# Optimization experiments

Hardware: AMD Instinct MI355X
Metric: run time of the kernel (lower is better)

The kernel has to match this reference:

```python
import jax, jax.numpy as jnp
import numpy as np

# Model dims (match init_kwargs)
E, D, H, K = 8, 512, 1024, 2   # num_experts, input/output dim, hidden dim, top_k
B, S = 4, 2048                 # batch, seq_len


def setup_inputs() -> dict:
    key = jax.random.key(0)
    ks = jax.random.split(key, 5)
    sd = lambda fan: np.float32(1.0 / np.sqrt(fan))
    return {
        "x": jax.random.normal(ks[0], (B, S, D), jnp.float32),
        "gate_w": jax.random.normal(ks[1], (D, E), jnp.float32) * sd(D),
        "gate_b": jnp.zeros((E,), jnp.float32),
        "w1": jax.random.normal(ks[2], (E, D, H), jnp.float32) * sd(D),
        "b1": jnp.zeros((E, H), jnp.float32),
        "w2": jax.random.normal(ks[3], (E, H, D), jnp.float32) * sd(H),
        "b2": jnp.zeros((E, D), jnp.float32),
    }


def reference(x, gate_w, gate_b, w1, b1, w2, b2):
    # x: [B, S, D]
    Bb, Ss, Dd = x.shape
    xf = x.reshape(-1, Dd)                              # [N, D], N = B*S

    # Router: softmax over experts, top-k, renormalize selected weights
    logits = xf @ gate_w + gate_b                        # [N, E]
    probs = jax.nn.softmax(logits, axis=-1)              # [N, E]
    top_w, top_i = jax.lax.top_k(probs, K)               # [N, K]
    top_w = top_w / top_w.sum(axis=-1, keepdims=True)

    # Per-token combine weight for each expert (0 if not routed).
    onehot = jax.nn.one_hot(top_i, E, dtype=probs.dtype)  # [N, K, E]
    combine = jnp.einsum("nke,nk->ne", onehot, top_w)     # [N, E]

    # Expert MLPs. Dropout is inactive at inference (identity).
    # h: [E, N, H]; GELU exact (torch nn.GELU default uses erf)
    h = jax.nn.gelu(jnp.einsum("nd,edh->enh", xf, w1) + b1[:, None, :],
                    approximate=False)
    y = jnp.einsum("enh,ehd->end", h, w2) + b2[:, None, :]  # [E, N, D]

    # Weighted combine: tokens not routed to expert e have combine[:, e] == 0.
    out = jnp.einsum("end,ne->nd", y, combine).reshape(Bb, Ss, Dd)
    return out, probs.reshape(Bb, Ss, E)
```

## Files before the change

kernel.cpp:

```cpp
#include <hip/hip_runtime.h>
#include <stdint.h>

#define N_TOK 8192
#define DIM   512
#define HID   1024
#define NE    8
#define NSLOT 16384
#define MAXSLOT 17408

typedef __attribute__((ext_vector_type(8))) short short8;
typedef __attribute__((ext_vector_type(4))) float f32x4;

#define W1T_OFF  0ull
#define W2T_OFF  8388608ull
#define H_OFF    16777216ull
#define Y_OFF    52428800ull
#define XBF_OFF  52428800ull
#define TOPI_OFF 70254592ull
#define TOPW_OFF 70320128ull
#define SLOT_OFF 70385664ull
#define ROWS_OFF 70451200ull
#define RW_OFF   70520832ull
#define CNT_OFF  70590464ull

__device__ __forceinline__ unsigned int f2bfu(float f) {
  union { float f; unsigned int i; } v; v.f = f;
  unsigned int u = v.i;
  return (u + 0x7FFFu + ((u >> 16) & 1u)) >> 16;
}
__device__ __forceinline__ float bf2f(unsigned int u) {
  union { unsigned int i; float f; } v; v.i = (u & 0xFFFFu) << 16; return v.f;
}
__device__ __forceinline__ float gelu_f(float x) {
  float x2 = x * x;
  float u = x * (1.59576912f + 0.07135481f * x2);
  float ez = __expf(-u);
  return x * __builtin_amdgcn_rcpf(1.0f + ez);
}
__device__ __forceinline__ void async16(void* lds, const void* g) {
  __builtin_amdgcn_global_load_lds(
      (const __attribute__((address_space(1))) unsigned int*)g,
      (__attribute__((address_space(3))) unsigned int*)lds, 16, 0, 0);
}

__global__ __launch_bounds__(256) void k_transpose(
    const float* __restrict__ w1, const float* __restrict__ w2,
    unsigned short* __restrict__ w1t, unsigned short* __restrict__ w2t) {
  __shared__ unsigned short tile[64][68];
  int b = blockIdx.x, tid = threadIdx.x;
  const float* src; unsigned short* dst; int R, C;
  if (b < 1024) { int e = b >> 7; int t = b & 127;
    src = w1 + (size_t)e * 524288; dst = w1t + (size_t)e * 524288; R = 512; C = 1024;
    int tr = t >> 4, tc = t & 15;
    src += (size_t)tr * 64 * C + tc * 64; dst += (size_t)tc * 64 * R + tr * 64;
  } else { b -= 1024; int e = b >> 7; int t = b & 127;
    src = w2 + (size_t)e * 524288; dst = w2t + (size_t)e * 524288; R = 1024; C = 512;
    int tr = t >> 3, tc = t & 7;
    src += (size_t)tr * 64 * C + tc * 64; dst += (size_t)tc * 64 * R + tr * 64;
  }
#pragma unroll
  for (int i = 0; i < 4; ++i) {
    int l = i * 256 + tid;
    int r = l >> 4, c4 = (l & 15) << 2;
    float4 v = *(const float4*)(src + (size_t)r * C + c4);
    tile[r][c4 + 0] = (unsigned short)f2bfu(v.x);
    tile[r][c4 + 1] = (unsigned short)f2bfu(v.y);
    tile[r][c4 + 2] = (unsigned short)f2bfu(v.z);
    tile[r][c4 + 3] = (unsigned short)f2bfu(v.w);
  }
  __syncthreads();
#pragma unroll
  for (int i = 0; i < 2; ++i) {
    int l = i * 256 + tid;
    int rr = l >> 3, c8 = (l & 7) << 3;
    ushort4 a, b2v;
    a.x = tile[c8 + 0][rr]; a.y = tile[c8 + 1][rr];
    a.z = tile[c8 + 2][rr]; a.w = tile[c8 + 3][rr];
    b2v.x = tile[c8 + 4][rr]; b2v.y = tile[c8 + 5][rr];
    b2v.z = tile[c8 + 6][rr]; b2v.w = tile[c8 + 7][rr];
    uint4 pk;
    pk.x = (unsigned int)a.x | ((unsigned int)a.y << 16);
    pk.y = (unsigned int)a.z | ((unsigned int)a.w << 16);
    pk.z = (unsigned int)b2v.x | ((unsigned int)b2v.y << 16);
    pk.w = (unsigned int)b2v.z | ((unsigned int)b2v.w << 16);
    *(uint4*)(dst + (size_t)rr * R + c8) = pk;
  }
}

__global__ __launch_bounds__(256) void k_router(
    const float* __restrict__ x, const float* __restrict__ gw,
    const float* __restrict__ gb, float* __restrict__ probs_out,
    int2* __restrict__ topi, float2* __restrict__ topw,
    unsigned short* __restrict__ xbf) {
  int wave = threadIdx.x >> 6, lane = threadIdx.x & 63;
  int n = blockIdx.x * 4 + wave;
  const float4* xr = (const float4*)(x + (size_t)n * DIM);
  float4 x0 = xr[lane * 2], x1 = xr[lane * 2 + 1];
  float xf[8] = {x0.x, x0.y, x0.z, x0.w, x1.x, x1.y, x1.z, x1.w};
  uint4 pa;
  pa.x = f2bfu(xf[0]) | (f2bfu(xf[1]) << 16);
  pa.y = f2bfu(xf[2]) | (f2bfu(xf[3]) << 16);
  pa.z = f2bfu(xf[4]) | (f2bfu(xf[5]) << 16);
  pa.w = f2bfu(xf[6]) | (f2bfu(xf[7]) << 16);
  *(uint4*)(xbf + (size_t)n * DIM + lane * 8) = pa;
  float acc[8] = {0.f,0.f,0.f,0.f,0.f,0.f,0.f,0.f};
  const float4* gwr = (const float4*)gw;
#pragma unroll
  for (int j = 0; j < 8; ++j) {
    int d = lane * 8 + j;
    float4 g0 = gwr[d * 2], g1 = gwr[d * 2 + 1];
    acc[0] += xf[j] * g0.x; acc[1] += xf[j] * g0.y; acc[2] += xf[j] * g0.z; acc[3] += xf[j] * g0.w;
    acc[4] += xf[j] * g1.x; acc[5] += xf[j] * g1.y; acc[6] += xf[j] * g1.z; acc[7] += xf[j] * g1.w;
  }
#pragma unroll
  for (int o = 1; o < 64; o <<= 1)
#pragma unroll
    for (int e = 0; e < 8; ++e) acc[e] += __shfl_xor(acc[e], o, 64);
  float p[8], mx = -1e30f, s = 0.f;
#pragma unroll
  for (int e = 0; e < 8; ++e) { p[e] = acc[e] + gb[e]; mx = fmaxf(mx, p[e]); }
#pragma unroll
  for (int e = 0; e < 8; ++e) { p[e] = __expf(p[e] - mx); s += p[e]; }
  float inv = 1.f / s;
#pragma unroll
  for (int e = 0; e < 8; ++e) p[e] *= inv;
  if (lane < 8) probs_out[(size_t)n * NE + lane] = p[lane];
  if (lane == 0) {
    int i0 = 0; float v0 = p[0];
#pragma unroll
    for (int e = 1; e < 8; ++e) if (p[e] > v0) { v0 = p[e]; i0 = e; }
    int i1 = -1; float v1 = -1.f;
#pragma unroll
    for (int e = 0; e < 8; ++e) if (e != i0 && p[e] > v1) { v1 = p[e]; i1 = e; }
    float sw = 1.f / (v0 + v1);
    topi[n] = make_int2(i0, i1);
    topw[n] = make_float2(v0 * sw, v1 * sw);
  }
}

__global__ __launch_bounds__(1024) void k_count(
    const int2* __restrict__ topi, int* __restrict__ meta, int* __restrict__ chunk_base,
    int* __restrict__ rows, float* __restrict__ rw) {
  __shared__ int ch[32][8];
  __shared__ int tot[8], poff_s[9], tiles_s[8];
  int t = threadIdx.x;
  int g = t >> 5;
  if (t < 256) ((int*)ch)[t] = 0;
  __syncthreads();
  int c[8] = {0,0,0,0,0,0,0,0};
  int base_tok = t * 8;
#pragma unroll
  for (int i = 0; i < 8; ++i) {
    int2 e = topi[base_tok + i];
#pragma unroll
    for (int k = 0; k < 8; ++k) c[k] += (e.x == k) + (e.y == k);
  }
#pragma unroll
  for (int k = 0; k < 8; ++k) if (c[k]) atomicAdd(&ch[g][k], c[k]);
  __syncthreads();
  if (t < 8) {
    int a = 0;
#pragma unroll
    for (int b = 0; b < 32; ++b) { int v = ch[b][t]; ch[b][t] = a; a += v; }
    tot[t] = a; meta[t] = a;
  }
  __syncthreads();
  if (t == 0) {
    int a = 0, ts = 0;
#pragma unroll
    for (int e = 0; e < 8; ++e) {
      int tiles = (tot[e] + 127) >> 7;
      poff_s[e] = a; tiles_s[e] = tiles;
      meta[16 + e] = a; meta[32 + e] = ts;
      a += tiles << 7; ts += tiles;
    }
    poff_s[8] = a; meta[24] = a; meta[40] = ts;
  }
  __syncthreads();
  if (t < 256) {
    int b = t >> 3, e = t & 7;
    chunk_base[t] = poff_s[e] + ch[b][e];
  }
#pragma unroll
  for (int e = 0; e < 8; ++e) {
    int padn = (tiles_s[e] << 7) - tot[e];
    if (t < padn) {
      int s = poff_s[e] + tot[e] + t;
      rows[s] = 0; rw[s] = 0.f;
    }
  }
}

__global__ __launch_bounds__(256) void k_assign(
    const int2* __restrict__ topi, const float2* __restrict__ topw,
    const int* __restrict__ chunk_base,
    int* __restrict__ rows, float* __restrict__ rw, int* __restrict__ slot_of) {
  __shared__ int lcnt[8];
  __shared__ int lbase[8];
  int t = threadIdx.x, b = blockIdx.x;
  if (t < 8) { lcnt[t] = 0; lbase[t] = chunk_base[b * 8 + t]; }
  __syncthreads();
  int n = b * 256 + t;
  int2 ei = topi[n]; float2 wv = topw[n];
  int r0 = atomicAdd(&lcnt[ei.x], 1);
  int r1 = atomicAdd(&lcnt[ei.y], 1);
  int s0 = lbase[ei.x] + r0;
  int s1 = lbase[ei.y] + r1;
  rows[s0] = n; rw[s0] = wv.x; slot_of[2 * n] = s0;
  rows[s1] = n; rw[s1] = wv.y; slot_of[2 * n + 1] = s1;
}

__global__ __launch_bounds__(256) void k_gemm1(
    const unsigned short* __restrict__ xbf, const unsigned short* __restrict__ w1t,
    const float* __restrict__ b1, const int* __restrict__ meta,
    const int* __restrict__ rows, unsigned short* __restrict__ h) {
  int t = blockIdx.y;
  if (t >= meta[40]) return;
  int e = 0;
#pragma unroll
  for (int i = 1; i < 8; ++i) if (t >= meta[32 + i]) e = i;
  int mt = t - meta[32 + e];
  int row0 = meta[16 + e] + (mt << 7);
  int nt = blockIdx.x;
  __shared__ __align__(16) unsigned short As[2][4096];
  __shared__ __align__(16) unsigned short Bs[2][4096];
  int tid = threadIdx.x;
  int wave = tid >> 6, lane = tid & 63;
  int wr = wave & 1, wc = wave >> 1;
  f32x4 acc[4][4] = {};
  const unsigned short* bBase = w1t + (size_t)e * HID * DIM + (size_t)(nt * 128) * DIM;

  const unsigned short* ga[2]; const unsigned short* gb[2];
#pragma unroll
  for (int j = 0; j < 2; ++j) {
    int s = j * 256 + tid;
    int r = s >> 2;
    int cg = ((s & 3) ^ ((r >> 1) & 3)) << 3;
    ga[j] = xbf + (size_t)rows[row0 + r] * DIM + cg;
    gb[j] = bBase + (size_t)r * DIM + cg;
  }
  int ldst = (wave * 64) * 8;

#pragma unroll
  for (int j = 0; j < 2; ++j) {
    async16(&As[0][j * 2048 + ldst], ga[j]);
    async16(&Bs[0][j * 2048 + ldst], gb[j]);
  }
  __syncthreads();

  for (int k0 = 0; k0 < DIM; k0 += 32) {
    int cur = (k0 >> 5) & 1, nxt = cur ^ 1;
    if (k0 + 32 < DIM) {
#pragma unroll
      for (int j = 0; j < 2; ++j) {
        async16(&As[nxt][j * 2048 + ldst], ga[j] + k0 + 32);
        async16(&Bs[nxt][j * 2048 + ldst], gb[j] + k0 + 32);
      }
    }
    {
      int ca = lane >> 4;
      short8 tf[4], wf[4];
#pragma unroll
      for (int am = 0; am < 4; ++am) {
        int ra = wr * 64 + am * 16 + (lane & 15);
        tf[am] = *(const short8*)&As[cur][(ra * 4 + (ca ^ ((ra >> 1) & 3))) * 8];
      }
#pragma unroll
      for (int an = 0; an < 4; ++an) {
        int rb = wc * 64 + an * 16 + (lane & 15);
        wf[an] = *(const short8*)&Bs[cur][(rb * 4 + (ca ^ ((rb >> 1) & 3))) * 8];
      }
#pragma unroll
      for (int an = 0; an < 4; ++an)
#pragma unroll
        for (int am = 0; am < 4; ++am)
          acc[an][am] = __builtin_amdgcn_mfma_f32_16x16x32_bf16(wf[an], tf[am], acc[an][am], 0, 0, 0);
    }
    __syncthreads();
  }
  int ml = lane & 15, q = lane >> 4;
#pragma unroll
  for (int am = 0; am < 4; ++am) {
    int slot_r = row0 + wr * 64 + am * 16 + ml;
    unsigned short* hrow = h + (size_t)slot_r * HID;
#pragma unroll
    for (int an = 0; an < 4; ++an) {
      int colb = nt * 128 + wc * 64 + an * 16 + q * 4;
      float4 bias = *(const float4*)&b1[e * HID + colb];
      f32x4 v = acc[an][am];
      float g0 = gelu_f(v[0] + bias.x);
      float g1 = gelu_f(v[1] + bias.y);
      float g2 = gelu_f(v[2] + bias.z);
      float g3 = gelu_f(v[3] + bias.w);
      uint2 pk;
      pk.x = f2bfu(g0) | (f2bfu(g1) << 16);
      pk.y = f2bfu(g2) | (f2bfu(g3) << 16);
      *(uint2*)(hrow + colb) = pk;
    }
  }
}

__global__ __launch_bounds__(256) void k_gemm2(
    const unsigned short* __restrict__ h, const unsigned short* __restrict__ w2t,
    const float* __restrict__ b2, const int* __restrict__ meta,
    const float* __restrict__ rw, unsigned short* __restrict__ y) {
  int t = blockIdx.y;
  if (t >= meta[40]) return;
  int e = 0;
#pragma unroll
  for (int i = 1; i < 8; ++i) if (t >= meta[32 + i]) e = i;
  int mt = t - meta[32 + e];
  int row0 = meta[16 + e] + (mt << 7);
  int nt = blockIdx.x;
  __shared__ __align__(16) unsigned short As[2][4096];
  __shared__ __align__(16) unsigned short Bs[2][4096];
  int tid = threadIdx.x;
  int wave = tid >> 6, lane = tid & 63;
  int wr = wave & 1, wc = wave >> 1;
  f32x4 acc[4][4] = {};
  const unsigned short* aBase = h + (size_t)row0 * HID;
  const unsigned short* bBase = w2t + (size_t)e * DIM * HID + (size_t)(nt * 128) * HID;

  const unsigned short* ga[2]; const unsigned short* gb[2];
#pragma unroll
  for (int j = 0; j < 2; ++j) {
    int s = j * 256 + tid;
    int r = s >> 2;
    int cg = ((s & 3) ^ ((r >> 1) & 3)) << 3;
    ga[j] = aBase + (size_t)r * HID + cg;
    gb[j] = bBase + (size_t)r * HID + cg;
  }
  int ldst = (wave * 64) * 8;

#pragma unroll
  for (int j = 0; j < 2; ++j) {
    async16(&As[0][j * 2048 + ldst], ga[j]);
    async16(&Bs[0][j * 2048 + ldst], gb[j]);
  }
  __syncthreads();

  for (int k0 = 0; k0 < HID; k0 += 32) {
    int cur = (k0 >> 5) & 1, nxt = cur ^ 1;
    if (k0 + 32 < HID) {
#pragma unroll
      for (int j = 0; j < 2; ++j) {
        async16(&As[nxt][j * 2048 + ldst], ga[j] + k0 + 32);
        async16(&Bs[nxt][j * 2048 + ldst], gb[j] + k0 + 32);
      }
    }
    {
      int ca = lane >> 4;
      short8 tf[4], wf[4];
#pragma unroll
      for (int am = 0; am < 4; ++am) {
        int ra = wr * 64 + am * 16 + (lane & 15);
        tf[am] = *(const short8*)&As[cur][(ra * 4 + (ca ^ ((ra >> 1) & 3))) * 8];
      }
#pragma unroll
      for (int an = 0; an < 4; ++an) {
        int rb = wc * 64 + an * 16 + (lane & 15);
        wf[an] = *(const short8*)&Bs[cur][(rb * 4 + (ca ^ ((rb >> 1) & 3))) * 8];
      }
#pragma unroll
      for (int an = 0; an < 4; ++an)
#pragma unroll
        for (int am = 0; am < 4; ++am)
          acc[an][am] = __builtin_amdgcn_mfma_f32_16x16x32_bf16(wf[an], tf[am], acc[an][am], 0, 0, 0);
    }
    __syncthreads();
  }
  int ml = lane & 15, q = lane >> 4;
#pragma unroll
  for (int am = 0; am < 4; ++am) {
    int slot_r = row0 + wr * 64 + am * 16 + ml;
    float w = rw[slot_r];
    unsigned short* yrow = y + (size_t)slot_r * DIM;
#pragma unroll
    for (int an = 0; an < 4; ++an) {
      int colb = nt * 128 + wc * 64 + an * 16 + q * 4;
      float4 bias = *(const float4*)&b2[e * DIM + colb];
      f32x4 v = acc[an][am];
      uint2 pk;
      pk.x = f2bfu((v[0] + bias.x) * w) | (f2bfu((v[1] + bias.y) * w) << 16);
      pk.y = f2bfu((v[2] + bias.z) * w) | (f2bfu((v[3] + bias.w) * w) << 16);
      *(uint2*)(yrow + colb) = pk;
    }
  }
}

__global__ __launch_bounds__(256) void k_combine(
    const unsigned short* __restrict__ y, const int* __restrict__ slot_of,
    float* __restrict__ out) {
  int t = blockIdx.x * 256 + threadIdx.x;
  int n = t >> 6, c = (t & 63) << 3;
  int s0 = slot_of[2 * n], s1 = slot_of[2 * n + 1];
  uint4 u0 = *(const uint4*)(y + (size_t)s0 * DIM + c);
  uint4 u1 = *(const uint4*)(y + (size_t)s1 * DIM + c);
  float4 o0, o1;
  o0.x = bf2f(u0.x) + bf2f(u1.x); o0.y = bf2f(u0.x >> 16) + bf2f(u1.x >> 16);
  o0.z = bf2f(u0.y) + bf2f(u1.y); o0.w = bf2f(u0.y >> 16) + bf2f(u1.y >> 16);
  o1.x = bf2f(u0.z) + bf2f(u1.z); o1.y = bf2f(u0.z >> 16) + bf2f(u1.z >> 16);
  o1.z = bf2f(u0.w) + bf2f(u1.w); o1.w = bf2f(u0.w >> 16) + bf2f(u1.w >> 16);
  *(float4*)(out + (size_t)n * DIM + c) = o0;
  *(float4*)(out + (size_t)n * DIM + c + 4) = o1;
}

extern "C" void kernel_launch(void* const* d_in, const int* in_sizes, int n_in,
                              void* d_out, int out_size, void* d_ws, size_t ws_size,
                              hipStream_t stream) {
  const float* x  = (const float*)d_in[0];
  const float* gw = (const float*)d_in[1];
  const float* gb = (const float*)d_in[2];
  const float* w1 = (const float*)d_in[3];
  const float* b1 = (const float*)d_in[4];
  const float* w2 = (const float*)d_in[5];
  const float* b2 = (const float*)d_in[6];
  float* out = (float*)d_out;
  char* ws = (char*)d_ws;

  unsigned short* w1t = (unsigned short*)(ws + W1T_OFF);
  unsigned short* w2t = (unsigned short*)(ws + W2T_OFF);
  unsigned short* h   = (unsigned short*)(ws + H_OFF);
  unsigned short* y   = (unsigned short*)(ws + Y_OFF);
  unsigned short* xbf = (unsigned short*)(ws + XBF_OFF);
  int2*   topi    = (int2*)(ws + TOPI_OFF);
  float2* topw    = (float2*)(ws + TOPW_OFF);
  int*    slot_of = (int*)(ws + SLOT_OFF);
  int*    rows    = (int*)(ws + ROWS_OFF);
  float*  rw      = (float*)(ws + RW_OFF);
  int*    meta    = (int*)(ws + CNT_OFF);
  int*    chunk_base = meta + 64;
  float*  probs   = out + (size_t)N_TOK * DIM;

  k_transpose<<<dim3(2048), dim3(256), 0, stream>>>(w1, w2, w1t, w2t);
  k_router   <<<dim3(2048), dim3(256), 0, stream>>>(x, gw, gb, probs, topi, topw, xbf);
  k_count    <<<dim3(1),    dim3(1024), 0, stream>>>(topi, meta, chunk_base, rows, rw);
  k_assign   <<<dim3(32),   dim3(256), 0, stream>>>(topi, topw, chunk_base, rows, rw, slot_of);
  k_gemm1    <<<dim3(8, 136), dim3(256), 0, stream>>>(xbf, w1t, b1, meta, rows, h);
  k_gemm2    <<<dim3(4, 136), dim3(256), 0, stream>>>(h, w2t, b2, meta, rw, y);
  k_combine  <<<dim3(2048), dim3(256), 0, stream>>>(y, slot_of, out);
}
```

Before: 210.0 us.

## Use three-stage LDS pipeline with vmcnt waits in both expert GEMMs

```diff
diff --git a/kernel.cpp b/kernel.cpp
--- a/kernel.cpp
+++ b/kernel.cpp
@@ -222,8 +222,8 @@
   int mt = t - meta[32 + e];
   int row0 = meta[16 + e] + (mt << 7);
   int nt = blockIdx.x;
-  __shared__ __align__(16) unsigned short As[2][4096];
-  __shared__ __align__(16) unsigned short Bs[2][4096];
+  __shared__ __align__(16) unsigned short As[3][4096];
+  __shared__ __align__(16) unsigned short Bs[3][4096];
   int tid = threadIdx.x;
   int wave = tid >> 6, lane = tid & 63;
   int wr = wave & 1, wc = wave >> 1;
@@ -242,43 +242,46 @@
   int ldst = (wave * 64) * 8;
 
 #pragma unroll
-  for (int j = 0; j < 2; ++j) {
-    async16(&As[0][j * 2048 + ldst], ga[j]);
-    async16(&Bs[0][j * 2048 + ldst], gb[j]);
-  }
-  __syncthreads();
-
-  for (int k0 = 0; k0 < DIM; k0 += 32) {
-    int cur = (k0 >> 5) & 1, nxt = cur ^ 1;
-    if (k0 + 32 < DIM) {
+  for (int s = 0; s < 2; ++s)
+#pragma unroll
+    for (int j = 0; j < 2; ++j) {
+      async16(&As[s][j * 2048 + ldst], ga[j] + s * 32);
+      async16(&Bs[s][j * 2048 + ldst], gb[j] + s * 32);
+    }
+
+  int ml = lane & 15, q = lane >> 4;
+#pragma unroll
+  for (int k = 0; k < 16; ++k) {
+    if (k < 15) { asm volatile("s_waitcnt vmcnt(4)" ::: "memory"); }
+    else        { asm volatile("s_waitcnt vmcnt(0)" ::: "memory"); }
+    __builtin_amdgcn_s_barrier();
+    if (k < 14) {
+      int stb = (k + 2) % 3;
+      int koff = (k + 2) * 32;
 #pragma unroll
       for (int j = 0; j < 2; ++j) {
-        async16(&As[nxt][j * 2048 + ldst], ga[j] + k0 + 32);
-        async16(&Bs[nxt][j * 2048 + ldst], gb[j] + k0 + 32);
+        async16(&As[stb][j * 2048 + ldst], ga[j] + koff);
+        async16(&Bs[stb][j * 2048 + ldst], gb[j] + koff);
       }
     }
-    {
-      int ca = lane >> 4;
-      short8 tf[4], wf[4];
-#pragma unroll
-      for (int am = 0; am < 4; ++am) {
-        int ra = wr * 64 + am * 16 + (lane & 15);
-        tf[am] = *(const short8*)&As[cur][(ra * 4 + (ca ^ ((ra >> 1) & 3))) * 8];
-      }
-#pragma unroll
-      for (int an = 0; an < 4; ++an) {
-        int rb = wc * 64 + an * 16 + (lane & 15);
-        wf[an] = *(const short8*)&Bs[cur][(rb * 4 + (ca ^ ((rb >> 1) & 3))) * 8];
-      }
-#pragma unroll
-      for (int an = 0; an < 4; ++an)
-#pragma unroll
-        for (int am = 0; am < 4; ++am)
-          acc[an][am] = __builtin_amdgcn_mfma_f32_16x16x32_bf16(wf[an], tf[am], acc[an][am], 0, 0, 0);
-    }
-    __syncthreads();
-  }
-  int ml = lane & 15, q = lane >> 4;
+    int cur = k % 3;
+    short8 tf[4], wf[4];
+#pragma unroll
+    for (int am = 0; am < 4; ++am) {
+      int ra = wr * 64 + am * 16 + ml;
+      tf[am] = *(const short8*)&As[cur][(ra * 4 + (q ^ ((ra >> 1) & 3))) * 8];
+    }
+#pragma unroll
+    for (int an = 0; an < 4; ++an) {
+      int rb = wc * 64 + an * 16 + ml;
+      wf[an] = *(const short8*)&Bs[cur][(rb * 4 + (q ^ ((rb >> 1) & 3))) * 8];
+    }
+#pragma unroll
+    for (int an = 0; an < 4; ++an)
+#pragma unroll
+      for (int am = 0; am < 4; ++am)
+        acc[an][am] = __builtin_amdgcn_mfma_f32_16x16x32_bf16(wf[an], tf[am], acc[an][am], 0, 0, 0);
+  }
 #pragma unroll
   for (int am = 0; am < 4; ++am) {
     int slot_r = row0 + wr * 64 + am * 16 + ml;
@@ -312,8 +315,8 @@
   int mt = t - meta[32 + e];
   int row0 = meta[16 + e] + (mt << 7);
   int nt = blockIdx.x;
-  __shared__ __align__(16) unsigned short As[2][4096];
-  __shared__ __align__(16) unsigned short Bs[2][4096];
+  __shared__ __align__(16) unsigned short As[3][4096];
+  __shared__ __align__(16) unsigned short Bs[3][4096];
   int tid = threadIdx.x;
   int wave = tid >> 6, lane = tid & 63;
   int wr = wave & 1, wc = wave >> 1;
@@ -333,43 +336,46 @@
   int ldst = (wave * 64) * 8;
 
 #pragma unroll
-  for (int j = 0; j < 2; ++j) {
-    async16(&As[0][j * 2048 + ldst], ga[j]);
-    async16(&Bs[0][j * 2048 + ldst], gb[j]);
-  }
-  __syncthreads();
-
-  for (int k0 = 0; k0 < HID; k0 += 32) {
-    int cur = (k0 >> 5) & 1, nxt = cur ^ 1;
-    if (k0 + 32 < HID) {
+  for (int s = 0; s < 2; ++s)
+#pragma unroll
+    for (int j = 0; j < 2; ++j) {
+      async16(&As[s][j * 2048 + ldst], ga[j] + s * 32);
+      async16(&Bs[s][j * 2048 + ldst], gb[j] + s * 32);
+    }
+
+  int ml = lane & 15, q = lane >> 4;
+#pragma unroll
+  for (int k = 0; k < 32; ++k) {
+    if (k < 31) { asm volatile("s_waitcnt vmcnt(4)" ::: "memory"); }
+    else        { asm volatile("s_waitcnt vmcnt(0)" ::: "memory"); }
+    __builtin_amdgcn_s_barrier();
+    if (k < 30) {
+      int stb = (k + 2) % 3;
+      int koff = (k + 2) * 32;
 #pragma unroll
       for (int j = 0; j < 2; ++j) {
-        async16(&As[nxt][j * 2048 + ldst], ga[j] + k0 + 32);
-        async16(&Bs[nxt][j * 2048 + ldst], gb[j] + k0 + 32);
+        async16(&As[stb][j * 2048 + ldst], ga[j] + koff);
+        async16(&Bs[stb][j * 2048 + ldst], gb[j] + koff);
       }
     }
-    {
-      int ca = lane >> 4;
-      short8 tf[4], wf[4];
-#pragma unroll
-      for (int am = 0; am < 4; ++am) {
-        int ra = wr * 64 + am * 16 + (lane & 15);
-        tf[am] = *(const short8*)&As[cur][(ra * 4 + (ca ^ ((ra >> 1) & 3))) * 8];
-      }
-#pragma unroll
-      for (int an = 0; an < 4; ++an) {
-        int rb = wc * 64 + an * 16 + (lane & 15);
-        wf[an] = *(const short8*)&Bs[cur][(rb * 4 + (ca ^ ((rb >> 1) & 3))) * 8];
-      }
-#pragma unroll
-      for (int an = 0; an < 4; ++an)
-#pragma unroll
-        for (int am = 0; am < 4; ++am)
-          acc[an][am] = __builtin_amdgcn_mfma_f32_16x16x32_bf16(wf[an], tf[am], acc[an][am], 0, 0, 0);
-    }
-    __syncthreads();
-  }
-  int ml = lane & 15, q = lane >> 4;
+    int cur = k % 3;
+    short8 tf[4], wf[4];
+#pragma unroll
+    for (int am = 0; am < 4; ++am) {
+      int ra = wr * 64 + am * 16 + ml;
+      tf[am] = *(const short8*)&As[cur][(ra * 4 + (q ^ ((ra >> 1) & 3))) * 8];
+    }
+#pragma unroll
+    for (int an = 0; an < 4; ++an) {
+      int rb = wc * 64 + an * 16 + ml;
+      wf[an] = *(const short8*)&Bs[cur][(rb * 4 + (q ^ ((rb >> 1) & 3))) * 8];
+    }
+#pragma unroll
+    for (int an = 0; an < 4; ++an)
+#pragma unroll
+      for (int am = 0; am < 4; ++am)
+        acc[an][am] = __builtin_amdgcn_mfma_f32_16x16x32_bf16(wf[an], tf[am], acc[an][am], 0, 0, 0);
+  }
 #pragma unroll
   for (int am = 0; am < 4; ++am) {
     int slot_r = row0 + wr * 64 + am * 16 + ml;
```

Result: no change. 211.9 us (+0.9%).

## Use 256-row M tiles, 8 waves, and 5-buffer 3-deep async LDS pipeline

Applied to the files above, without the earlier changes.

```diff
diff --git a/kernel.cpp b/kernel.cpp
--- a/kernel.cpp
+++ b/kernel.cpp
@@ -6,7 +6,7 @@
 #define HID   1024
 #define NE    8
 #define NSLOT 16384
-#define MAXSLOT 17408
+#define MAXSLOT 18432
 
 typedef __attribute__((ext_vector_type(8))) short short8;
 typedef __attribute__((ext_vector_type(4))) float f32x4;
@@ -14,14 +14,14 @@
 #define W1T_OFF  0ull
 #define W2T_OFF  8388608ull
 #define H_OFF    16777216ull
-#define Y_OFF    52428800ull
-#define XBF_OFF  52428800ull
-#define TOPI_OFF 70254592ull
-#define TOPW_OFF 70320128ull
-#define SLOT_OFF 70385664ull
-#define ROWS_OFF 70451200ull
-#define RW_OFF   70520832ull
-#define CNT_OFF  70590464ull
+#define Y_OFF    54525952ull
+#define XBF_OFF  54525952ull
+#define TOPI_OFF 73400320ull
+#define TOPW_OFF 73465856ull
+#define SLOT_OFF 73531392ull
+#define ROWS_OFF 73596928ull
+#define RW_OFF   73670656ull
+#define CNT_OFF  73744384ull
 
 __device__ __forceinline__ unsigned int f2bfu(float f) {
   union { float f; unsigned int i; } v; v.f = f;
@@ -169,10 +169,10 @@
     int a = 0, ts = 0;
 #pragma unroll
     for (int e = 0; e < 8; ++e) {
-      int tiles = (tot[e] + 127) >> 7;
+      int tiles = (tot[e] + 255) >> 8;
       poff_s[e] = a; tiles_s[e] = tiles;
       meta[16 + e] = a; meta[32 + e] = ts;
-      a += tiles << 7; ts += tiles;
+      a += tiles << 8; ts += tiles;
     }
     poff_s[8] = a; meta[24] = a; meta[40] = ts;
   }
@@ -183,7 +183,7 @@
   }
 #pragma unroll
   for (int e = 0; e < 8; ++e) {
-    int padn = (tiles_s[e] << 7) - tot[e];
+    int padn = (tiles_s[e] << 8) - tot[e];
     if (t < padn) {
       int s = poff_s[e] + tot[e] + t;
       rows[s] = 0; rw[s] = 0.f;
@@ -210,7 +210,7 @@
   rows[s1] = n; rw[s1] = wv.y; slot_of[2 * n + 1] = s1;
 }
 
-__global__ __launch_bounds__(256) void k_gemm1(
+__global__ __launch_bounds__(512, 2) void k_gemm1(
     const unsigned short* __restrict__ xbf, const unsigned short* __restrict__ w1t,
     const float* __restrict__ b1, const int* __restrict__ meta,
     const int* __restrict__ rows, unsigned short* __restrict__ h) {
@@ -220,65 +220,71 @@
 #pragma unroll
   for (int i = 1; i < 8; ++i) if (t >= meta[32 + i]) e = i;
   int mt = t - meta[32 + e];
-  int row0 = meta[16 + e] + (mt << 7);
+  int row0 = meta[16 + e] + (mt << 8);
   int nt = blockIdx.x;
-  __shared__ __align__(16) unsigned short As[2][4096];
-  __shared__ __align__(16) unsigned short Bs[2][4096];
+  __shared__ __align__(16) unsigned short As[5][8192];
+  __shared__ __align__(16) unsigned short Bs[5][4096];
   int tid = threadIdx.x;
   int wave = tid >> 6, lane = tid & 63;
-  int wr = wave & 1, wc = wave >> 1;
+  int wr = wave & 3, wc = wave >> 2;
   f32x4 acc[4][4] = {};
   const unsigned short* bBase = w1t + (size_t)e * HID * DIM + (size_t)(nt * 128) * DIM;
 
-  const unsigned short* ga[2]; const unsigned short* gb[2];
-#pragma unroll
-  for (int j = 0; j < 2; ++j) {
-    int s = j * 256 + tid;
-    int r = s >> 2;
-    int cg = ((s & 3) ^ ((r >> 1) & 3)) << 3;
-    ga[j] = xbf + (size_t)rows[row0 + r] * DIM + cg;
-    gb[j] = bBase + (size_t)r * DIM + cg;
-  }
-  int ldst = (wave * 64) * 8;
-
-#pragma unroll
-  for (int j = 0; j < 2; ++j) {
-    async16(&As[0][j * 2048 + ldst], ga[j]);
-    async16(&Bs[0][j * 2048 + ldst], gb[j]);
-  }
-  __syncthreads();
-
-  for (int k0 = 0; k0 < DIM; k0 += 32) {
-    int cur = (k0 >> 5) & 1, nxt = cur ^ 1;
-    if (k0 + 32 < DIM) {
-#pragma unroll
-      for (int j = 0; j < 2; ++j) {
-        async16(&As[nxt][j * 2048 + ldst], ga[j] + k0 + 32);
-        async16(&Bs[nxt][j * 2048 + ldst], gb[j] + k0 + 32);
-      }
-    }
-    {
-      int ca = lane >> 4;
-      short8 tf[4], wf[4];
-#pragma unroll
-      for (int am = 0; am < 4; ++am) {
-        int ra = wr * 64 + am * 16 + (lane & 15);
-        tf[am] = *(const short8*)&As[cur][(ra * 4 + (ca ^ ((ra >> 1) & 3))) * 8];
-      }
-#pragma unroll
-      for (int an = 0; an < 4; ++an) {
-        int rb = wc * 64 + an * 16 + (lane & 15);
-        wf[an] = *(const short8*)&Bs[cur][(rb * 4 + (ca ^ ((rb >> 1) & 3))) * 8];
-      }
-#pragma unroll
-      for (int an = 0; an < 4; ++an)
-#pragma unroll
-        for (int am = 0; am < 4; ++am)
-          acc[an][am] = __builtin_amdgcn_mfma_f32_16x16x32_bf16(wf[an], tf[am], acc[an][am], 0, 0, 0);
-    }
-    __syncthreads();
-  }
+  const unsigned short *ga0, *ga1, *gbp;
+  {
+    int s0 = tid;        int r0g = s0 >> 2; int c0 = ((s0 & 3) ^ ((r0g >> 1) & 3)) << 3;
+    ga0 = xbf + (size_t)rows[row0 + r0g] * DIM + c0;
+    int s1 = 512 + tid;  int r1g = s1 >> 2; int c1 = ((s1 & 3) ^ ((r1g >> 1) & 3)) << 3;
+    ga1 = xbf + (size_t)rows[row0 + r1g] * DIM + c1;
+    int sb = tid;        int rbg = sb >> 2; int cb = ((sb & 3) ^ ((rbg >> 1) & 3)) << 3;
+    gbp = bBase + (size_t)rbg * DIM + cb;
+  }
+  int la0 = (wave * 64) * 8;
+  int la1 = (512 + wave * 64) * 8;
+  int lb  = (wave * 64) * 8;
+
+#define STAGE1(buf, kt) do { \
+    async16(&As[buf][la0], ga0 + (kt) * 32); \
+    async16(&As[buf][la1], ga1 + (kt) * 32); \
+    async16(&Bs[buf][lb],  gbp + (kt) * 32); \
+  } while (0)
+
+  STAGE1(0, 0); STAGE1(1, 1); STAGE1(2, 2);
+  asm volatile("s_waitcnt vmcnt(6)" ::: "memory");
+  __builtin_amdgcn_s_barrier();
+
   int ml = lane & 15, q = lane >> 4;
+  int offA[4], offB[4];
+#pragma unroll
+  for (int am = 0; am < 4; ++am) { int ra = wr * 64 + am * 16 + ml; offA[am] = (ra * 4 + (q ^ ((ra >> 1) & 3))) * 8; }
+#pragma unroll
+  for (int an = 0; an < 4; ++an) { int rb = wc * 64 + an * 16 + ml; offB[an] = (rb * 4 + (q ^ ((rb >> 1) & 3))) * 8; }
+
+#pragma unroll
+  for (int kt = 0; kt < 16; ++kt) {
+    int buf = kt % 5;
+    if (kt + 3 < 16) STAGE1((kt + 3) % 5, kt + 3);
+    short8 tf[4], wf[4];
+#pragma unroll
+    for (int am = 0; am < 4; ++am) tf[am] = *(const short8*)&As[buf][offA[am]];
+#pragma unroll
+    for (int an = 0; an < 4; ++an) wf[an] = *(const short8*)&Bs[buf][offB[an]];
+    __builtin_amdgcn_s_setprio(1);
+#pragma unroll
+    for (int an = 0; an < 4; ++an)
+#pragma unroll
+      for (int am = 0; am < 4; ++am)
+        acc[an][am] = __builtin_amdgcn_mfma_f32_16x16x32_bf16(wf[an], tf[am], acc[an][am], 0, 0, 0);
+    __builtin_amdgcn_s_setprio(0);
+    if (kt < 15) {
+      if (kt <= 12)      asm volatile("s_waitcnt vmcnt(6)" ::: "memory");
+      else if (kt == 13) asm volatile("s_waitcnt vmcnt(3)" ::: "memory");
+      else               asm volatile("s_waitcnt vmcnt(0)" ::: "memory");
+      __builtin_amdgcn_s_barrier();
+    }
+  }
+#undef STAGE1
+
 #pragma unroll
   for (int am = 0; am < 4; ++am) {
     int slot_r = row0 + wr * 64 + am * 16 + ml;
@@ -300,7 +306,7 @@
   }
 }
 
-__global__ __launch_bounds__(256) void k_gemm2(
+__global__ __launch_bounds__(512, 2) void k_gemm2(
     const unsigned short* __restrict__ h, const unsigned short* __restrict__ w2t,
     const float* __restrict__ b2, const int* __restrict__ meta,
     const float* __restrict__ rw, unsigned short* __restrict__ y) {
@@ -310,66 +316,72 @@
 #pragma unroll
   for (int i = 1; i < 8; ++i) if (t >= meta[32 + i]) e = i;
   int mt = t - meta[32 + e];
-  int row0 = meta[16 + e] + (mt << 7);
+  int row0 = meta[16 + e] + (mt << 8);
   int nt = blockIdx.x;
-  __shared__ __align__(16) unsigned short As[2][4096];
-  __shared__ __align__(16) unsigned short Bs[2][4096];
+  __shared__ __align__(16) unsigned short As[5][8192];
+  __shared__ __align__(16) unsigned short Bs[5][4096];
   int tid = threadIdx.x;
   int wave = tid >> 6, lane = tid & 63;
-  int wr = wave & 1, wc = wave >> 1;
+  int wr = wave & 3, wc = wave >> 2;
   f32x4 acc[4][4] = {};
   const unsigned short* aBase = h + (size_t)row0 * HID;
   const unsigned short* bBase = w2t + (size_t)e * DIM * HID + (size_t)(nt * 128) * HID;
 
-  const unsigned short* ga[2]; const unsigned short* gb[2];
-#pragma unroll
-  for (int j = 0; j < 2; ++j) {
-    int s = j * 256 + tid;
-    int r = s >> 2;
-    int cg = ((s & 3) ^ ((r >> 1) & 3)) << 3;
-    ga[j] = aBase + (size_t)r * HID + cg;
-    gb[j] = bBase + (size_t)r * HID + cg;
-  }
-  int ldst = (wave * 64) * 8;
-
-#pragma unroll
-  for (int j = 0; j < 2; ++j) {
-    async16(&As[0][j * 2048 + ldst], ga[j]);
-    async16(&Bs[0][j * 2048 + ldst], gb[j]);
-  }
-  __syncthreads();
-
-  for (int k0 = 0; k0 < HID; k0 += 32) {
-    int cur = (k0 >> 5) & 1, nxt = cur ^ 1;
-    if (k0 + 32 < HID) {
-#pragma unroll
-      for (int j = 0; j < 2; ++j) {
-        async16(&As[nxt][j * 2048 + ldst], ga[j] + k0 + 32);
-        async16(&Bs[nxt][j * 2048 + ldst], gb[j] + k0 + 32);
-      }
-    }
-    {
-      int ca = lane >> 4;
-      short8 tf[4], wf[4];
-#pragma unroll
-      for (int am = 0; am < 4; ++am) {
-        int ra = wr * 64 + am * 16 + (lane & 15);
-        tf[am] = *(const short8*)&As[cur][(ra * 4 + (ca ^ ((ra >> 1) & 3))) * 8];
-      }
-#pragma unroll
-      for (int an = 0; an < 4; ++an) {
-        int rb = wc * 64 + an * 16 + (lane & 15);
-        wf[an] = *(const short8*)&Bs[cur][(rb * 4 + (ca ^ ((rb >> 1) & 3))) * 8];
-      }
-#pragma unroll
-      for (int an = 0; an < 4; ++an)
-#pragma unroll
-        for (int am = 0; am < 4; ++am)
-          acc[an][am] = __builtin_amdgcn_mfma_f32_16x16x32_bf16(wf[an], tf[am], acc[an][am], 0, 0, 0);
-    }
-    __syncthreads();
-  }
+  const unsigned short *ga0, *ga1, *gbp;
+  {
+    int s0 = tid;        int r0g = s0 >> 2; int c0 = ((s0 & 3) ^ ((r0g >> 1) & 3)) << 3;
+    ga0 = aBase + (size_t)r0g * HID + c0;
+    int s1 = 512 + tid;  int r1g = s1 >> 2; int c1 = ((s1 & 3) ^ ((r1g >> 1) & 3)) << 3;
+    ga1 = aBase + (size_t)r1g * HID + c1;
+    int sb = tid;        int rbg = sb >> 2; int cb = ((sb & 3) ^ ((rbg >> 1) & 3)) << 3;
+    gbp = bBase + (size_t)rbg * HID + cb;
+  }
+  int la0 = (wave * 64) * 8;
+  int la1 = (512 + wave * 64) * 8;
+  int lb  = (wave * 64) * 8;
+
+#define STAGE2(buf, kt) do { \
+    async16(&As[buf][la0], ga0 + (kt) * 32); \
+    async16(&As[buf][la1], ga1 + (kt) * 32); \
+    async16(&Bs[buf][lb],  gbp + (kt) * 32); \
+  } while (0)
+
+  STAGE2(0, 0); STAGE2(1, 1); STAGE2(2, 2);
+  asm volatile("s_waitcnt vmcnt(6)" ::: "memory");
+  __builtin_amdgcn_s_barrier();
+
   int ml = lane & 15, q = lane >> 4;
+  int offA[4], offB[4];
+#pragma unroll
+  for (int am = 0; am < 4; ++am) { int ra = wr * 64 + am * 16 + ml; offA[am] = (ra * 4 + (q ^ ((ra >> 1) & 3))) * 8; }
+#pragma unroll
+  for (int an = 0; an < 4; ++an) { int rb = wc * 64 + an * 16 + ml; offB[an] = (rb * 4 + (q ^ ((rb >> 1) & 3))) * 8; }
+
+#pragma unroll
+  for (int kt = 0; kt < 32; ++kt) {
+    int buf = kt % 5;
+    if (kt + 3 < 32) STAGE2((kt + 3) % 5, kt + 3);
+    short8 tf[4], wf[4];
+#pragma unroll
+    for (int am = 0; am < 4; ++am) tf[am] = *(const short8*)&As[buf][offA[am]];
+#pragma unroll
+    for (int an = 0; an < 4; ++an) wf[an] = *(const short8*)&Bs[buf][offB[an]];
+    __builtin_amdgcn_s_setprio(1);
+#pragma unroll
+    for (int an = 0; an < 4; ++an)
+#pragma unroll
+      for (int am = 0; am < 4; ++am)
+        acc[an][am] = __builtin_amdgcn_mfma_f32_16x16x32_bf16(wf[an], tf[am], acc[an][am], 0, 0, 0);
+    __builtin_amdgcn_s_setprio(0);
+    if (kt < 31) {
+      if (kt <= 28)      asm volatile("s_waitcnt vmcnt(6)" ::: "memory");
+      else if (kt == 29) asm volatile("s_waitcnt vmcnt(3)" ::: "memory");
+      else               asm volatile("s_waitcnt vmcnt(0)" ::: "memory");
+      __builtin_amdgcn_s_barrier();
+    }
+  }
+#undef STAGE2
+
 #pragma unroll
   for (int am = 0; am < 4; ++am) {
     int slot_r = row0 + wr * 64 + am * 16 + ml;
@@ -436,7 +448,7 @@
   k_router   <<<dim3(2048), dim3(256), 0, stream>>>(x, gw, gb, probs, topi, topw, xbf);
   k_count    <<<dim3(1),    dim3(1024), 0, stream>>>(topi, meta, chunk_base, rows, rw);
   k_assign   <<<dim3(32),   dim3(256), 0, stream>>>(topi, topw, chunk_base, rows, rw, slot_of);
-  k_gemm1    <<<dim3(8, 136), dim3(256), 0, stream>>>(xbf, w1t, b1, meta, rows, h);
-  k_gemm2    <<<dim3(4, 136), dim3(256), 0, stream>>>(h, w2t, b2, meta, rw, y);
+  k_gemm1    <<<dim3(8, 71), dim3(512), 0, stream>>>(xbf, w1t, b1, meta, rows, h);
+  k_gemm2    <<<dim3(4, 71), dim3(512), 0, stream>>>(h, w2t, b2, meta, rw, y);
   k_combine  <<<dim3(2048), dim3(256), 0, stream>>>(y, slot_of, out);
 }
```

Result: slower. 230.0 us (+9.5%).

## Merge prep kernels, fuse count/assign, and remap GEMM blocks across XCDs

Applied to the files above, without the earlier changes.

```diff
diff --git a/kernel.cpp b/kernel.cpp
--- a/kernel.cpp
+++ b/kernel.cpp
@@ -43,120 +43,134 @@
       (__attribute__((address_space(3))) unsigned int*)lds, 16, 0, 0);
 }
 
-__global__ __launch_bounds__(256) void k_transpose(
+__global__ __launch_bounds__(256) void k_prep(
     const float* __restrict__ w1, const float* __restrict__ w2,
-    unsigned short* __restrict__ w1t, unsigned short* __restrict__ w2t) {
-  __shared__ unsigned short tile[64][68];
-  int b = blockIdx.x, tid = threadIdx.x;
-  const float* src; unsigned short* dst; int R, C;
-  if (b < 1024) { int e = b >> 7; int t = b & 127;
-    src = w1 + (size_t)e * 524288; dst = w1t + (size_t)e * 524288; R = 512; C = 1024;
-    int tr = t >> 4, tc = t & 15;
-    src += (size_t)tr * 64 * C + tc * 64; dst += (size_t)tc * 64 * R + tr * 64;
-  } else { b -= 1024; int e = b >> 7; int t = b & 127;
-    src = w2 + (size_t)e * 524288; dst = w2t + (size_t)e * 524288; R = 1024; C = 512;
-    int tr = t >> 3, tc = t & 7;
-    src += (size_t)tr * 64 * C + tc * 64; dst += (size_t)tc * 64 * R + tr * 64;
-  }
-#pragma unroll
-  for (int i = 0; i < 4; ++i) {
-    int l = i * 256 + tid;
-    int r = l >> 4, c4 = (l & 15) << 2;
-    float4 v = *(const float4*)(src + (size_t)r * C + c4);
-    tile[r][c4 + 0] = (unsigned short)f2bfu(v.x);
-    tile[r][c4 + 1] = (unsigned short)f2bfu(v.y);
-    tile[r][c4 + 2] = (unsigned short)f2bfu(v.z);
-    tile[r][c4 + 3] = (unsigned short)f2bfu(v.w);
-  }
-  __syncthreads();
-#pragma unroll
-  for (int i = 0; i < 2; ++i) {
-    int l = i * 256 + tid;
-    int rr = l >> 3, c8 = (l & 7) << 3;
-    ushort4 a, b2v;
-    a.x = tile[c8 + 0][rr]; a.y = tile[c8 + 1][rr];
-    a.z = tile[c8 + 2][rr]; a.w = tile[c8 + 3][rr];
-    b2v.x = tile[c8 + 4][rr]; b2v.y = tile[c8 + 5][rr];
-    b2v.z = tile[c8 + 6][rr]; b2v.w = tile[c8 + 7][rr];
-    uint4 pk;
-    pk.x = (unsigned int)a.x | ((unsigned int)a.y << 16);
-    pk.y = (unsigned int)a.z | ((unsigned int)a.w << 16);
-    pk.z = (unsigned int)b2v.x | ((unsigned int)b2v.y << 16);
-    pk.w = (unsigned int)b2v.z | ((unsigned int)b2v.w << 16);
-    *(uint4*)(dst + (size_t)rr * R + c8) = pk;
-  }
-}
-
-__global__ __launch_bounds__(256) void k_router(
+    unsigned short* __restrict__ w1t, unsigned short* __restrict__ w2t,
     const float* __restrict__ x, const float* __restrict__ gw,
     const float* __restrict__ gb, float* __restrict__ probs_out,
     int2* __restrict__ topi, float2* __restrict__ topw,
     unsigned short* __restrict__ xbf) {
-  int wave = threadIdx.x >> 6, lane = threadIdx.x & 63;
-  int n = blockIdx.x * 4 + wave;
-  const float4* xr = (const float4*)(x + (size_t)n * DIM);
-  float4 x0 = xr[lane * 2], x1 = xr[lane * 2 + 1];
-  float xf[8] = {x0.x, x0.y, x0.z, x0.w, x1.x, x1.y, x1.z, x1.w};
-  uint4 pa;
-  pa.x = f2bfu(xf[0]) | (f2bfu(xf[1]) << 16);
-  pa.y = f2bfu(xf[2]) | (f2bfu(xf[3]) << 16);
-  pa.z = f2bfu(xf[4]) | (f2bfu(xf[5]) << 16);
-  pa.w = f2bfu(xf[6]) | (f2bfu(xf[7]) << 16);
-  *(uint4*)(xbf + (size_t)n * DIM + lane * 8) = pa;
-  float acc[8] = {0.f,0.f,0.f,0.f,0.f,0.f,0.f,0.f};
-  const float4* gwr = (const float4*)gw;
-#pragma unroll
-  for (int j = 0; j < 8; ++j) {
-    int d = lane * 8 + j;
-    float4 g0 = gwr[d * 2], g1 = gwr[d * 2 + 1];
-    acc[0] += xf[j] * g0.x; acc[1] += xf[j] * g0.y; acc[2] += xf[j] * g0.z; acc[3] += xf[j] * g0.w;
-    acc[4] += xf[j] * g1.x; acc[5] += xf[j] * g1.y; acc[6] += xf[j] * g1.z; acc[7] += xf[j] * g1.w;
-  }
-#pragma unroll
-  for (int o = 1; o < 64; o <<= 1)
-#pragma unroll
-    for (int e = 0; e < 8; ++e) acc[e] += __shfl_xor(acc[e], o, 64);
-  float p[8], mx = -1e30f, s = 0.f;
-#pragma unroll
-  for (int e = 0; e < 8; ++e) { p[e] = acc[e] + gb[e]; mx = fmaxf(mx, p[e]); }
-#pragma unroll
-  for (int e = 0; e < 8; ++e) { p[e] = __expf(p[e] - mx); s += p[e]; }
-  float inv = 1.f / s;
-#pragma unroll
-  for (int e = 0; e < 8; ++e) p[e] *= inv;
-  if (lane < 8) probs_out[(size_t)n * NE + lane] = p[lane];
-  if (lane == 0) {
-    int i0 = 0; float v0 = p[0];
-#pragma unroll
-    for (int e = 1; e < 8; ++e) if (p[e] > v0) { v0 = p[e]; i0 = e; }
-    int i1 = -1; float v1 = -1.f;
-#pragma unroll
-    for (int e = 0; e < 8; ++e) if (e != i0 && p[e] > v1) { v1 = p[e]; i1 = e; }
-    float sw = 1.f / (v0 + v1);
-    topi[n] = make_int2(i0, i1);
-    topw[n] = make_float2(v0 * sw, v1 * sw);
-  }
-}
-
-__global__ __launch_bounds__(1024) void k_count(
-    const int2* __restrict__ topi, int* __restrict__ meta, int* __restrict__ chunk_base,
-    int* __restrict__ rows, float* __restrict__ rw) {
+  __shared__ unsigned short tile[64][68];
+  int tid = threadIdx.x;
+  if (blockIdx.x < 2048) {
+    int b = blockIdx.x;
+    const float* src; unsigned short* dst; int R, C;
+    if (b < 1024) { int e = b >> 7; int t = b & 127;
+      src = w1 + (size_t)e * 524288; dst = w1t + (size_t)e * 524288; R = 512; C = 1024;
+      int tr = t >> 4, tc = t & 15;
+      src += (size_t)tr * 64 * C + tc * 64; dst += (size_t)tc * 64 * R + tr * 64;
+    } else { b -= 1024; int e = b >> 7; int t = b & 127;
+      src = w2 + (size_t)e * 524288; dst = w2t + (size_t)e * 524288; R = 1024; C = 512;
+      int tr = t >> 3, tc = t & 7;
+      src += (size_t)tr * 64 * C + tc * 64; dst += (size_t)tc * 64 * R + tr * 64;
+    }
+#pragma unroll
+    for (int i = 0; i < 4; ++i) {
+      int l = i * 256 + tid;
+      int r = l >> 4, c4 = (l & 15) << 2;
+      float4 v = *(const float4*)(src + (size_t)r * C + c4);
+      tile[r][c4 + 0] = (unsigned short)f2bfu(v.x);
+      tile[r][c4 + 1] = (unsigned short)f2bfu(v.y);
+      tile[r][c4 + 2] = (unsigned short)f2bfu(v.z);
+      tile[r][c4 + 3] = (unsigned short)f2bfu(v.w);
+    }
+    __syncthreads();
+#pragma unroll
+    for (int i = 0; i < 2; ++i) {
+      int l = i * 256 + tid;
+      int rr = l >> 3, c8 = (l & 7) << 3;
+      ushort4 a, b2v;
+      a.x = tile[c8 + 0][rr]; a.y = tile[c8 + 1][rr];
+      a.z = tile[c8 + 2][rr]; a.w = tile[c8 + 3][rr];
+      b2v.x = tile[c8 + 4][rr]; b2v.y = tile[c8 + 5][rr];
+      b2v.z = tile[c8 + 6][rr]; b2v.w = tile[c8 + 7][rr];
+      uint4 pk;
+      pk.x = (unsigned int)a.x | ((unsigned int)a.y << 16);
+      pk.y = (unsigned int)a.z | ((unsigned int)a.w << 16);
+      pk.z = (unsigned int)b2v.x | ((unsigned int)b2v.y << 16);
+      pk.w = (unsigned int)b2v.z | ((unsigned int)b2v.w << 16);
+      *(uint4*)(dst + (size_t)rr * R + c8) = pk;
+    }
+  } else {
+    int wave = tid >> 6, lane = tid & 63;
+    int n = (blockIdx.x - 2048) * 4 + wave;
+    const float4* xr = (const float4*)(x + (size_t)n * DIM);
+    float4 x0 = xr[lane * 2], x1 = xr[lane * 2 + 1];
+    float xf[8] = {x0.x, x0.y, x0.z, x0.w, x1.x, x1.y, x1.z, x1.w};
+    uint4 pa;
+    pa.x = f2bfu(xf[0]) | (f2bfu(xf[1]) << 16);
+    pa.y = f2bfu(xf[2]) | (f2bfu(xf[3]) << 16);
+    pa.z = f2bfu(xf[4]) | (f2bfu(xf[5]) << 16);
+    pa.w = f2bfu(xf[6]) | (f2bfu(xf[7]) << 16);
+    *(uint4*)(xbf + (size_t)n * DIM + lane * 8) = pa;
+    float acc[8] = {0.f,0.f,0.f,0.f,0.f,0.f,0.f,0.f};
+    const float4* gwr = (const float4*)gw;
+#pragma unroll
+    for (int j = 0; j < 8; ++j) {
+      int d = lane * 8 + j;
+      float4 g0 = gwr[d * 2], g1 = gwr[d * 2 + 1];
+      acc[0] += xf[j] * g0.x; acc[1] += xf[j] * g0.y; acc[2] += xf[j] * g0.z; acc[3] += xf[j] * g0.w;
+      acc[4] += xf[j] * g1.x; acc[5] += xf[j] * g1.y; acc[6] += xf[j] * g1.z; acc[7] += xf[j] * g1.w;
+    }
+#pragma unroll
+    for (int o = 1; o < 64; o <<= 1)
+#pragma unroll
+      for (int e = 0; e < 8; ++e) acc[e] += __shfl_xor(acc[e], o, 64);
+    float p[8], mx = -1e30f, s = 0.f;
+#pragma unroll
+    for (int e = 0; e < 8; ++e) { p[e] = acc[e] + gb[e]; mx = fmaxf(mx, p[e]); }
+#pragma unroll
+    for (int e = 0; e < 8; ++e) { p[e] = __expf(p[e] - mx); s += p[e]; }
+    float inv = 1.f / s;
+#pragma unroll
+    for (int e = 0; e < 8; ++e) p[e] *= inv;
+    if (lane < 8) probs_out[(size_t)n * NE + lane] = p[lane];
+    if (lane == 0) {
+      int i0 = 0; float v0 = p[0];
+#pragma unroll
+      for (int e = 1; e < 8; ++e) if (p[e] > v0) { v0 = p[e]; i0 = e; }
+      int i1 = -1; float v1 = -1.f;
+#pragma unroll
+      for (int e = 0; e < 8; ++e) if (e != i0 && p[e] > v1) { v1 = p[e]; i1 = e; }
+      float sw = 1.f / (v0 + v1);
+      topi[n] = make_int2(i0, i1);
+      topw[n] = make_float2(v0 * sw, v1 * sw);
+    }
+  }
+}
+
+__global__ __launch_bounds__(1024) void k_countassign(
+    const int2* __restrict__ topi, const float2* __restrict__ topw,
+    int* __restrict__ meta, int* __restrict__ rows, float* __restrict__ rw,
+    int* __restrict__ slot_of) {
   __shared__ int ch[32][8];
   __shared__ int tot[8], poff_s[9], tiles_s[8];
-  int t = threadIdx.x;
-  int g = t >> 5;
+  __shared__ int sm_off[1024 * 8];
+  int t = threadIdx.x, g = t >> 5;
   if (t < 256) ((int*)ch)[t] = 0;
   __syncthreads();
+  int2 te[8]; float2 tw[8];
   int c[8] = {0,0,0,0,0,0,0,0};
   int base_tok = t * 8;
 #pragma unroll
   for (int i = 0; i < 8; ++i) {
-    int2 e = topi[base_tok + i];
-#pragma unroll
-    for (int k = 0; k < 8; ++k) c[k] += (e.x == k) + (e.y == k);
+    te[i] = topi[base_tok + i];
+    tw[i] = topw[base_tok + i];
+#pragma unroll
+    for (int k = 0; k < 8; ++k) c[k] += (te[i].x == k) + (te[i].y == k);
   }
 #pragma unroll
   for (int k = 0; k < 8; ++k) if (c[k]) atomicAdd(&ch[g][k], c[k]);
+#pragma unroll
+  for (int k = 0; k < 8; ++k) {
+    int s = c[k];
+#pragma unroll
+    for (int d = 1; d < 32; d <<= 1) {
+      int u = __shfl_up(s, d, 32);
+      if ((t & 31) >= d) s += u;
+    }
+    sm_off[t * 8 + k] = s - c[k];
+  }
   __syncthreads();
   if (t < 8) {
     int a = 0;
@@ -177,9 +191,16 @@
     poff_s[8] = a; meta[24] = a; meta[40] = ts;
   }
   __syncthreads();
-  if (t < 256) {
-    int b = t >> 3, e = t & 7;
-    chunk_base[t] = poff_s[e] + ch[b][e];
+#pragma unroll
+  for (int i = 0; i < 8; ++i) {
+    int n = base_tok + i;
+    int e0 = te[i].x, e1 = te[i].y;
+    int o0 = sm_off[t * 8 + e0]++;
+    int s0 = poff_s[e0] + ch[g][e0] + o0;
+    int o1 = sm_off[t * 8 + e1]++;
+    int s1 = poff_s[e1] + ch[g][e1] + o1;
+    rows[s0] = n; rw[s0] = tw[i].x; slot_of[2 * n] = s0;
+    rows[s1] = n; rw[s1] = tw[i].y; slot_of[2 * n + 1] = s1;
   }
 #pragma unroll
   for (int e = 0; e < 8; ++e) {
@@ -191,37 +212,20 @@
   }
 }
 
-__global__ __launch_bounds__(256) void k_assign(
-    const int2* __restrict__ topi, const float2* __restrict__ topw,
-    const int* __restrict__ chunk_base,
-    int* __restrict__ rows, float* __restrict__ rw, int* __restrict__ slot_of) {
-  __shared__ int lcnt[8];
-  __shared__ int lbase[8];
-  int t = threadIdx.x, b = blockIdx.x;
-  if (t < 8) { lcnt[t] = 0; lbase[t] = chunk_base[b * 8 + t]; }
-  __syncthreads();
-  int n = b * 256 + t;
-  int2 ei = topi[n]; float2 wv = topw[n];
-  int r0 = atomicAdd(&lcnt[ei.x], 1);
-  int r1 = atomicAdd(&lcnt[ei.y], 1);
-  int s0 = lbase[ei.x] + r0;
-  int s1 = lbase[ei.y] + r1;
-  rows[s0] = n; rw[s0] = wv.x; slot_of[2 * n] = s0;
-  rows[s1] = n; rw[s1] = wv.y; slot_of[2 * n + 1] = s1;
-}
-
 __global__ __launch_bounds__(256) void k_gemm1(
     const unsigned short* __restrict__ xbf, const unsigned short* __restrict__ w1t,
     const float* __restrict__ b1, const int* __restrict__ meta,
     const int* __restrict__ rows, unsigned short* __restrict__ h) {
-  int t = blockIdx.y;
+  int lin = blockIdx.x;
+  int xcd = lin & 7, j = lin >> 3;
+  int t = xcd * 17 + (j >> 3);
+  int nt = j & 7;
   if (t >= meta[40]) return;
   int e = 0;
 #pragma unroll
   for (int i = 1; i < 8; ++i) if (t >= meta[32 + i]) e = i;
   int mt = t - meta[32 + e];
   int row0 = meta[16 + e] + (mt << 7);
-  int nt = blockIdx.x;
   __shared__ __align__(16) unsigned short As[2][4096];
   __shared__ __align__(16) unsigned short Bs[2][4096];
   int tid = threadIdx.x;
@@ -232,19 +236,19 @@
 
   const unsigned short* ga[2]; const unsigned short* gb[2];
 #pragma unroll
-  for (int j = 0; j < 2; ++j) {
-    int s = j * 256 + tid;
+  for (int jj = 0; jj < 2; ++jj) {
+    int s = jj * 256 + tid;
     int r = s >> 2;
     int cg = ((s & 3) ^ ((r >> 1) & 3)) << 3;
-    ga[j] = xbf + (size_t)rows[row0 + r] * DIM + cg;
-    gb[j] = bBase + (size_t)r * DIM + cg;
+    ga[jj] = xbf + (size_t)rows[row0 + r] * DIM + cg;
+    gb[jj] = bBase + (size_t)r * DIM + cg;
   }
   int ldst = (wave * 64) * 8;
 
 #pragma unroll
-  for (int j = 0; j < 2; ++j) {
-    async16(&As[0][j * 2048 + ldst], ga[j]);
-    async16(&Bs[0][j * 2048 + ldst], gb[j]);
+  for (int jj = 0; jj < 2; ++jj) {
+    async16(&As[0][jj * 2048 + ldst], ga[jj]);
+    async16(&Bs[0][jj * 2048 + ldst], gb[jj]);
   }
   __syncthreads();
 
@@ -252,9 +256,9 @@
     int cur = (k0 >> 5) & 1, nxt = cur ^ 1;
     if (k0 + 32 < DIM) {
 #pragma unroll
-      for (int j = 0; j < 2; ++j) {
-        async16(&As[nxt][j * 2048 + ldst], ga[j] + k0 + 32);
-        async16(&Bs[nxt][j * 2048 + ldst], gb[j] + k0 + 32);
+      for (int jj = 0; jj < 2; ++jj) {
+        async16(&As[nxt][jj * 2048 + ldst], ga[jj] + k0 + 32);
+        async16(&Bs[nxt][jj * 2048 + ldst], gb[jj] + k0 + 32);
       }
     }
     {
@@ -304,14 +308,16 @@
     const unsigned short* __restrict__ h, const unsigned short* __restrict__ w2t,
     const float* __restrict__ b2, const int* __restrict__ meta,
     const float* __restrict__ rw, unsigned short* __restrict__ y) {
-  int t = blockIdx.y;
+  int lin = blockIdx.x;
+  int xcd = lin & 7, j = lin >> 3;
+  int t = xcd * 17 + (j >> 2);
+  int nt = j & 3;
   if (t >= meta[40]) return;
   int e = 0;
 #pragma unroll
   for (int i = 1; i < 8; ++i) if (t >= meta[32 + i]) e = i;
   int mt = t - meta[32 + e];
   int row0 = meta[16 + e] + (mt << 7);
-  int nt = blockIdx.x;
   __shared__ __align__(16) unsigned short As[2][4096];
   __shared__ __align__(16) unsigned short Bs[2][4096];
   int tid = threadIdx.x;
@@ -323,19 +329,19 @@
 
   const unsigned short* ga[2]; const unsigned short* gb[2];
 #pragma unroll
-  for (int j = 0; j < 2; ++j) {
-    int s = j * 256 + tid;
+  for (int jj = 0; jj < 2; ++jj) {
+    int s = jj * 256 + tid;
     int r = s >> 2;
     int cg = ((s & 3) ^ ((r >> 1) & 3)) << 3;
-    ga[j] = aBase + (size_t)r * HID + cg;
-    gb[j] = bBase + (size_t)r * HID + cg;
+    ga[jj] = aBase + (size_t)r * HID + cg;
+    gb[jj] = bBase + (size_t)r * HID + cg;
   }
   int ldst = (wave * 64) * 8;
 
 #pragma unroll
-  for (int j = 0; j < 2; ++j) {
-    async16(&As[0][j * 2048 + ldst], ga[j]);
-    async16(&Bs[0][j * 2048 + ldst], gb[j]);
+  for (int jj = 0; jj < 2; ++jj) {
+    async16(&As[0][jj * 2048 + ldst], ga[jj]);
+    async16(&Bs[0][jj * 2048 + ldst], gb[jj]);
   }
   __syncthreads();
 
@@ -343,9 +349,9 @@
     int cur = (k0 >> 5) & 1, nxt = cur ^ 1;
     if (k0 + 32 < HID) {
 #pragma unroll
-      for (int j = 0; j < 2; ++j) {
-        async16(&As[nxt][j * 2048 + ldst], ga[j] + k0 + 32);
-        async16(&Bs[nxt][j * 2048 + ldst], gb[j] + k0 + 32);
+      for (int jj = 0; jj < 2; ++jj) {
+        async16(&As[nxt][jj * 2048 + ldst], ga[jj] + k0 + 32);
+        async16(&Bs[nxt][jj * 2048 + ldst], gb[jj] + k0 + 32);
       }
     }
     {
@@ -429,14 +435,12 @@
   int*    rows    = (int*)(ws + ROWS_OFF);
   float*  rw      = (float*)(ws + RW_OFF);
   int*    meta    = (int*)(ws + CNT_OFF);
-  int*    chunk_base = meta + 64;
   float*  probs   = out + (size_t)N_TOK * DIM;
 
-  k_transpose<<<dim3(2048), dim3(256), 0, stream>>>(w1, w2, w1t, w2t);
-  k_router   <<<dim3(2048), dim3(256), 0, stream>>>(x, gw, gb, probs, topi, topw, xbf);
-  k_count    <<<dim3(1),    dim3(1024), 0, stream>>>(topi, meta, chunk_base, rows, rw);
-  k_assign   <<<dim3(32),   dim3(256), 0, stream>>>(topi, topw, chunk_base, rows, rw, slot_of);
-  k_gemm1    <<<dim3(8, 136), dim3(256), 0, stream>>>(xbf, w1t, b1, meta, rows, h);
-  k_gemm2    <<<dim3(4, 136), dim3(256), 0, stream>>>(h, w2t, b2, meta, rw, y);
-  k_combine  <<<dim3(2048), dim3(256), 0, stream>>>(y, slot_of, out);
-}
+  k_prep       <<<dim3(4096), dim3(256),  0, stream>>>(w1, w2, w1t, w2t,
+                                                       x, gw, gb, probs, topi, topw, xbf);
+  k_countassign<<<dim3(1),    dim3(1024), 0, stream>>>(topi, topw, meta, rows, rw, slot_of);
+  k_gemm1      <<<dim3(1088), dim3(256),  0, stream>>>(xbf, w1t, b1, meta, rows, h);
+  k_gemm2      <<<dim3(544),  dim3(256),  0, stream>>>(h, w2t, b2, meta, rw, y);
+  k_combine    <<<dim3(2048), dim3(256),  0, stream>>>(y, slot_of, out);
+}
```

Measured after the change: 207.2 us. About the same (-1.3%).
